# Performance work log

Hardware: AMD Instinct MI355X
Metric: run time of the kernel (lower is better)

Reference implementation:

```python
import jax, jax.numpy as jnp
import numpy as np

S, H, NH, I = 4096, 2048, 16, 5504
HD = H // NH
EPS = 1e-6
ROPE_BASE = 10000.0


def setup_inputs() -> dict:
    key = jax.random.key(0)
    ks = jax.random.split(key, 10)
    sc = lambda fan_in: 1.0 / np.sqrt(fan_in)
    return {
        "x": jax.random.normal(ks[0], (S, H), jnp.float32),
        "wq": jax.random.normal(ks[1], (H, H), jnp.float32) * sc(H),
        "wk": jax.random.normal(ks[2], (H, H), jnp.float32) * sc(H),
        "wv": jax.random.normal(ks[3], (H, H), jnp.float32) * sc(H),
        "wo": jax.random.normal(ks[4], (H, H), jnp.float32) * sc(H),
        "w_gate": jax.random.normal(ks[5], (H, I), jnp.float32) * sc(H),
        "w_up": jax.random.normal(ks[6], (H, I), jnp.float32) * sc(H),
        "w_down": jax.random.normal(ks[7], (I, H), jnp.float32) * sc(I),
        "g1": jnp.ones((H,), jnp.float32),
        "g2": jnp.ones((H,), jnp.float32),
    }


def _rmsnorm(x, g):
    var = jnp.mean(x * x, axis=-1, keepdims=True)
    return x * jax.lax.rsqrt(var + EPS) * g


def _rope(x):
    # x: [S, NH, HD]; classic interleaved-pair rotation applied per position.
    pos = jnp.arange(S, dtype=jnp.float32)
    inv_freq = 1.0 / (ROPE_BASE ** (jnp.arange(0, HD, 2, dtype=jnp.float32) / HD))
    ang = pos[:, None] * inv_freq[None, :]              # [S, HD/2]
    cos = jnp.cos(ang)[:, None, :]                      # [S, 1, HD/2]
    sin = jnp.sin(ang)[:, None, :]
    xe = x[..., 0::2]
    xo = x[..., 1::2]
    out = jnp.stack([xe * cos - xo * sin, xe * sin + xo * cos], axis=-1)
    return out.reshape(x.shape)


def _block(x, wq, wk, wv, wo, w_gate, w_up, w_down, g1, g2):
    # --- attention sublayer ---
    h = _rmsnorm(x, g1)
    q = _rope((h @ wq).reshape(S, NH, HD))
    k = _rope((h @ wk).reshape(S, NH, HD))
    v = (h @ wv).reshape(S, NH, HD)
    scores = jnp.einsum("snd,tnd->nst", q, k) / np.sqrt(HD).astype(np.float32)
    causal = jnp.tril(jnp.ones((S, S), bool))
    scores = jnp.where(causal[None], scores, jnp.finfo(scores.dtype).min)
    probs = jax.nn.softmax(scores, axis=-1)
    attn = jnp.einsum("nst,tnd->snd", probs, v).reshape(S, H)
    x = x + attn @ wo
    # --- MLP sublayer (SwiGLU) ---
    h = _rmsnorm(x, g2)
    mlp = (jax.nn.silu(h @ w_gate) * (h @ w_up)) @ w_down
    return x + mlp


def reference(x, wq, wk, wv, wo, w_gate, w_up, w_down, g1, g2):
    return _block(x, wq, wk, wv, wo, w_gate, w_up, w_down, g1, g2)
```

## Files before the change

### kernel.cpp

```cpp
#include <hip/hip_runtime.h>
#include <stdint.h>

constexpr int SEQ  = 4096;
constexpr int HID  = 2048;
constexpr int NHEAD = 16;
constexpr int HDIM = 128;
constexpr int INTER = 5504;
constexpr int IPAD  = 5632;

using u16 = unsigned short;
typedef __bf16 bf16x8 __attribute__((ext_vector_type(8)));
typedef float  f32x4  __attribute__((ext_vector_type(4)));
typedef u16    u16x4  __attribute__((ext_vector_type(4)));
typedef u16    u16x8  __attribute__((ext_vector_type(8)));

__device__ __forceinline__ u16 f2bf(float f) {
  union { float f; unsigned u; } v; v.f = f;
  return (u16)((v.u + 0x7fffu + ((v.u >> 16) & 1u)) >> 16);
}
__device__ __forceinline__ float bf2f(u16 u) {
  union { unsigned u; float f; } v; v.u = ((unsigned)u) << 16;
  return v.f;
}

__device__ __forceinline__ void gl16(const u16* g, u16* l) {
  u16* gg = const_cast<u16*>(g);
  __builtin_amdgcn_global_load_lds(
      (__attribute__((address_space(1))) u16*)gg,
      (__attribute__((address_space(3))) u16*)l, 16, 0, 0);
}

__device__ __forceinline__ f32x4 mfma16(bf16x8 a, bf16x8 b, f32x4 c) {
  return __builtin_amdgcn_mfma_f32_16x16x32_bf16(a, b, c, 0, 0, 0);
}

__global__ __launch_bounds__(256)
void fill_k(float* __restrict__ o, float v, int n) {
  int i = blockIdx.x * 256 + threadIdx.x;
  if (i < n) o[i] = v;
}

__global__ __launch_bounds__(256)
void rmsnorm_k(const float* __restrict__ x, const float* __restrict__ g,
               u16* __restrict__ o) {
  const int row = blockIdx.x, t = threadIdx.x;
  const float4* xr = (const float4*)(x + (size_t)row * HID);
  float4 a = xr[t * 2], b = xr[t * 2 + 1];
  float ss = a.x*a.x + a.y*a.y + a.z*a.z + a.w*a.w
           + b.x*b.x + b.y*b.y + b.z*b.z + b.w*b.w;
  #pragma unroll
  for (int m = 32; m; m >>= 1) ss += __shfl_xor(ss, m);
  __shared__ float red[4];
  if ((t & 63) == 0) red[t >> 6] = ss;
  __syncthreads();
  const float inv = rsqrtf((red[0]+red[1]+red[2]+red[3]) * (1.0f/HID) + 1e-6f);
  float vals[8] = {a.x,a.y,a.z,a.w,b.x,b.y,b.z,b.w};
  const int base = t * 8;
  u16x8 w;
  #pragma unroll
  for (int i = 0; i < 8; ++i) w[i] = f2bf(vals[i] * inv * g[base + i]);
  *(u16x8*)(o + (size_t)row * HID + base) = w;
}

__global__ __launch_bounds__(256)
void wtrans_k(const float* __restrict__ in, u16* __restrict__ out,
              int ldin, int ldout, int Rin, int Cin) {
  __shared__ float tile[32][33];
  const int cb = blockIdx.x * 32, rb = blockIdx.y * 32;
  const int t = threadIdx.x;
  const int c = t >> 3, r4 = (t & 7) * 4;
  if (rb >= Rin || cb >= Cin) {
    u16x4 z = {0, 0, 0, 0};
    *(u16x4*)(out + (size_t)(cb + c) * ldout + rb + r4) = z;
    return;
  }
  const int r = t >> 3, c4 = (t & 7) * 4;
  float4 v = *(const float4*)(in + (size_t)(rb + r) * ldin + cb + c4);
  tile[r][c4] = v.x; tile[r][c4+1] = v.y; tile[r][c4+2] = v.z; tile[r][c4+3] = v.w;
  __syncthreads();
  u16x4 o;
  #pragma unroll
  for (int i = 0; i < 4; ++i) o[i] = f2bf(tile[r4 + i][c]);
  *(u16x4*)(out + (size_t)(cb + c) * ldout + rb + r4) = o;
}

__global__ __launch_bounds__(256)
void vtrans_k(const u16* __restrict__ v, u16* __restrict__ vt) {
  __shared__ u16 tile[32][36];
  const int s0 = blockIdx.x * 32, d0 = blockIdx.y * 32, n = blockIdx.z;
  const int t = threadIdx.x;
  const int r = t >> 3, c4 = (t & 7) * 4;
  u16x4 in = *(const u16x4*)(v + (size_t)(s0 + r) * HID + n * HDIM + d0 + c4);
  tile[r][c4] = in[0]; tile[r][c4+1] = in[1]; tile[r][c4+2] = in[2]; tile[r][c4+3] = in[3];
  __syncthreads();
  const int d = t >> 3, s4 = (t & 7) * 4;
  u16x4 o;
  #pragma unroll
  for (int i = 0; i < 4; ++i) o[i] = tile[s4 + i][d];
  *(u16x4*)(vt + ((size_t)n * HDIM + d0 + d) * SEQ + s0 + s4) = o;
}

__global__ __launch_bounds__(256)
void rope_k(u16* __restrict__ x) {
  const int idx = blockIdx.x * 256 + threadIdx.x;
  const int i  = idx & 63;
  const int sn = idx >> 6;
  const int s  = sn >> 4;
  const size_t base = (size_t)sn * HDIM + 2 * i;
  const float xe = bf2f(x[base]), xo = bf2f(x[base + 1]);
  const float inv_freq = exp2f(-(float)i * (13.287712379549449f / 64.0f));
  const float ang = (float)s * inv_freq;
  float sv, cv;
  sincosf(ang, &sv, &cv);
  x[base]     = f2bf(xe * cv - xo * sv);
  x[base + 1] = f2bf(xe * sv + xo * cv);
}

template<int EPI>
__global__ __launch_bounds__(512, 2)
void gemm256(const u16* __restrict__ A, const u16* __restrict__ B,
             void* C, const void* extra, int M, int N, int K) {
  __shared__ __align__(16) u16 As[2][2][256 * 32];
  __shared__ __align__(16) u16 Bs[2][2][256 * 32];
  const int tid = threadIdx.x;
  const int w = tid >> 6, lane = tid & 63;
  const int l15 = lane & 15, g = lane >> 4;
  const int wr = w >> 2, wc = w & 3;
  const int m0 = blockIdx.y * 256, n0 = blockIdx.x * 256;
  const int NT = K >> 6;

  f32x4 acc[8][4] = {};

  const int srow0 = w * 32 + (lane >> 2);
  const int sgr   = (((lane & 3) ^ ((lane >> 2) & 3))) * 8;
  const u16* gA0 = A + (size_t)(m0 + srow0) * K + sgr;
  const u16* gB0 = B + (size_t)(n0 + srow0) * K + sgr;
  const size_t r16 = (size_t)16 * K;

#define STA(t, kh, buf) do { \
    const u16* s_ = gA0 + ((size_t)(t) * 64 + (kh) * 32); \
    u16* d_ = &As[buf][kh][w * 1024]; \
    gl16(s_, d_); gl16(s_ + r16, d_ + 512); \
  } while (0)
#define STB(t, kh, buf) do { \
    const u16* s_ = gB0 + ((size_t)(t) * 64 + (kh) * 32); \
    u16* d_ = &Bs[buf][kh][w * 1024]; \
    gl16(s_, d_); gl16(s_ + r16, d_ + 512); \
  } while (0)

  const int rsA = (wr * 128 + l15) * 32 + ((g ^ (l15 & 3)) * 8);
  const int rsB = (wc * 64  + l15) * 32 + ((g ^ (l15 & 3)) * 8);

  STB(0, 0, 0); STA(0, 0, 0); STB(0, 1, 0); STA(0, 1, 0);
  STB(1, 0, 1); STA(1, 0, 1);
  asm volatile("s_waitcnt vmcnt(8)" ::: "memory");
  __builtin_amdgcn_s_barrier();

  for (int T = 0; T < NT; ++T) {
    const int cur = T & 1, nxt = cur ^ 1;
    const int t1 = (T + 1 < NT) ? T + 1 : NT - 1;
    const int t2 = (T + 2 < NT) ? T + 2 : NT - 1;
    bf16x8 bfr[4], af[4];

    #pragma unroll
    for (int j = 0; j < 4; ++j) bfr[j] = *(const bf16x8*)&Bs[cur][0][rsB + j * 512];
    #pragma unroll
    for (int i = 0; i < 4; ++i) af[i] = *(const bf16x8*)&As[cur][0][rsA + i * 512];
    STB(t1, 1, nxt);
    __builtin_amdgcn_s_barrier();
    asm volatile("s_waitcnt lgkmcnt(0)" ::: "memory");
    __builtin_amdgcn_sched_barrier(0);
    __builtin_amdgcn_s_setprio(1);
    #pragma unroll
    for (int i = 0; i < 4; ++i)
      #pragma unroll
      for (int j = 0; j < 4; ++j) acc[i][j] = mfma16(af[i], bfr[j], acc[i][j]);
    __builtin_amdgcn_s_setprio(0);
    __builtin_amdgcn_s_barrier();

    #pragma unroll
    for (int i = 0; i < 4; ++i) af[i] = *(const bf16x8*)&As[cur][0][rsA + 2048 + i * 512];
    STA(t1, 1, nxt);
    asm volatile("s_waitcnt vmcnt(8)" ::: "memory");
    __builtin_amdgcn_s_barrier();
    asm volatile("s_waitcnt lgkmcnt(0)" ::: "memory");
    __builtin_amdgcn_sched_barrier(0);
    __builtin_amdgcn_s_setprio(1);
    #pragma unroll
    for (int i = 0; i < 4; ++i)
      #pragma unroll
      for (int j = 0; j < 4; ++j) acc[i + 4][j] = mfma16(af[i], bfr[j], acc[i + 4][j]);
    __builtin_amdgcn_s_setprio(0);
    __builtin_amdgcn_s_barrier();

    #pragma unroll
    for (int j = 0; j < 4; ++j) bfr[j] = *(const bf16x8*)&Bs[cur][1][rsB + j * 512];
    #pragma unroll
    for (int i = 0; i < 4; ++i) af[i] = *(const bf16x8*)&As[cur][1][rsA + i * 512];
    STB(t2, 0, cur);
    __builtin_amdgcn_s_barrier();
    asm volatile("s_waitcnt lgkmcnt(0)" ::: "memory");
    __builtin_amdgcn_sched_barrier(0);
    __builtin_amdgcn_s_setprio(1);
    #pragma unroll
    for (int i = 0; i < 4; ++i)
      #pragma unroll
      for (int j = 0; j < 4; ++j) acc[i][j] = mfma16(af[i], bfr[j], acc[i][j]);
    __builtin_amdgcn_s_setprio(0);
    __builtin_amdgcn_s_barrier();

    #pragma unroll
    for (int i = 0; i < 4; ++i) af[i] = *(const bf16x8*)&As[cur][1][rsA + 2048 + i * 512];
    STA(t2, 0, cur);
    asm volatile("s_waitcnt vmcnt(8)" ::: "memory");
    __builtin_amdgcn_s_barrier();
    asm volatile("s_waitcnt lgkmcnt(0)" ::: "memory");
    __builtin_amdgcn_sched_barrier(0);
    __builtin_amdgcn_s_setprio(1);
    #pragma unroll
    for (int i = 0; i < 4; ++i)
      #pragma unroll
      for (int j = 0; j < 4; ++j) acc[i + 4][j] = mfma16(af[i], bfr[j], acc[i + 4][j]);
    __builtin_amdgcn_s_setprio(0);
    __builtin_amdgcn_s_barrier();
  }
#undef STA
#undef STB

  #pragma unroll
  for (int i = 0; i < 8; ++i) {
    #pragma unroll
    for (int r = 0; r < 4; ++r) {
      const int row = m0 + wr * 128 + i * 16 + g * 4 + r;
      #pragma unroll
      for (int j = 0; j < 4; ++j) {
        const int col = n0 + wc * 64 + j * 16 + l15;
        const float v = acc[i][j][r];
        if constexpr (EPI == 0) {
          ((u16*)C)[(size_t)(col >> 11) * ((size_t)SEQ * HID)
                    + (size_t)row * HID + (col & 2047)] = f2bf(v);
        } else if constexpr (EPI == 1) {
          const size_t idx = (size_t)row * N + col;
          ((float*)C)[idx] = v + ((const float*)extra)[idx];
        } else if constexpr (EPI == 2) {
          const size_t idx = (size_t)row * N + col;
          const float upv = bf2f(((const u16*)extra)[idx]);
          ((u16*)C)[idx] = f2bf(v / (1.0f + __expf(-v)) * upv);
        } else {
          ((u16*)C)[(size_t)row * N + col] = f2bf(v);
        }
      }
    }
  }
}

__global__ __launch_bounds__(256)
void attn_k(const u16* __restrict__ q, const u16* __restrict__ k,
            const u16* __restrict__ vt, u16* __restrict__ o) {
  __shared__ __align__(16) u16 Ks[64 * 128];
  __shared__ __align__(16) u16 Vs[128 * 64];
  __shared__ __align__(16) u16 Ps[4 * 16 * 64];
  const int b = blockIdx.x;
  const int n    = ((b & 7) << 1) | ((b >> 3) & 1);
  const int qIdx = 63 - (b >> 4);
  const int q0   = qIdx * 64;
  const int tid = threadIdx.x;
  const int wave = tid >> 6, lane = tid & 63;
  const int l15 = lane & 15, g = lane >> 4;

  bf16x8 aq[4];
  {
    const u16* qp = q + (size_t)(q0 + wave*16 + l15) * HID + n * HDIM + g * 8;
    #pragma unroll
    for (int d = 0; d < 4; ++d) aq[d] = *(const bf16x8*)(qp + d * 32);
  }
  float mrow[4], lrow[4];
  #pragma unroll
  for (int r = 0; r < 4; ++r) { mrow[r] = -__builtin_inff(); lrow[r] = 0.0f; }
  f32x4 oacc[8] = {};

  const int kRow = tid >> 4;
  const int kCs  = (tid & 15) ^ (kRow & 7);
  const u16* kg = k + (size_t)kRow * HID + n * HDIM + kCs * 8;
  const int vRow = tid >> 3;
  const int vCs  = (tid & 7) ^ (vRow & 7);
  const u16* vg = vt + ((size_t)n * HDIM + vRow) * SEQ + vCs * 8;

  u16* PW = Ps + wave * 1024;
  const int rsw = (l15 & 7) << 3;
  const float C = 0.12751744f;

  const int nt = qIdx + 1;
  for (int it = 0; it < nt; ++it) {
    const int t0 = it * 64;
    #pragma unroll
    for (int s = 0; s < 4; ++s)
      gl16(kg + (size_t)(t0 + s*16) * HID, Ks + s*2048 + wave*512);
    #pragma unroll
    for (int s = 0; s < 4; ++s)
      gl16(vg + (size_t)(s*32) * SEQ + t0, Vs + s*2048 + wave*512);
    __syncthreads();

    f32x4 sc[4] = {};
    #pragma unroll
    for (int tb = 0; tb < 4; ++tb) {
      #pragma unroll
      for (int dd = 0; dd < 4; ++dd) {
        bf16x8 bk = *(const bf16x8*)(Ks + (tb*16 + l15)*128 + ((dd*32 + g*8) ^ rsw));
        sc[tb] = mfma16(aq[dd], bk, sc[tb]);
      }
    }

    float fex[4];
    #pragma unroll
    for (int r = 0; r < 4; ++r) {
      const int srow = q0 + wave*16 + g*4 + r;
      const int tt = t0 + l15;
      float v0 = sc[0][r], v1 = sc[1][r], v2 = sc[2][r], v3 = sc[3][r];
      if (tt      > srow) v0 = -__builtin_inff();
      if (tt + 16 > srow) v1 = -__builtin_inff();
      if (tt + 32 > srow) v2 = -__builtin_inff();
      if (tt + 48 > srow) v3 = -__builtin_inff();
      float mx = fmaxf(fmaxf(v0, v1), fmaxf(v2, v3));
      mx = fmaxf(mx, __shfl_xor(mx, 1));
      mx = fmaxf(mx, __shfl_xor(mx, 2));
      mx = fmaxf(mx, __shfl_xor(mx, 4));
      mx = fmaxf(mx, __shfl_xor(mx, 8));
      const float mnew = fmaxf(mrow[r], mx);
      const float f = exp2f((mrow[r] - mnew) * C);
      mrow[r] = mnew;
      const float p0 = exp2f((v0 - mnew) * C);
      const float p1 = exp2f((v1 - mnew) * C);
      const float p2 = exp2f((v2 - mnew) * C);
      const float p3 = exp2f((v3 - mnew) * C);
      float ps = (p0 + p1) + (p2 + p3);
      ps += __shfl_xor(ps, 1);
      ps += __shfl_xor(ps, 2);
      ps += __shfl_xor(ps, 4);
      ps += __shfl_xor(ps, 8);
      lrow[r] = lrow[r] * f + ps;
      fex[r] = f;
      const int prow = g*4 + r;
      const int psw = (prow & 7) << 3;
      PW[prow*64 + ( l15        ^ psw)] = f2bf(p0);
      PW[prow*64 + ((16 + l15)  ^ psw)] = f2bf(p1);
      PW[prow*64 + ((32 + l15)  ^ psw)] = f2bf(p2);
      PW[prow*64 + ((48 + l15)  ^ psw)] = f2bf(p3);
    }
    #pragma unroll
    for (int db = 0; db < 8; ++db)
      #pragma unroll
      for (int r = 0; r < 4; ++r) oacc[db][r] *= fex[r];

    bf16x8 ap0 = *(const bf16x8*)(PW + l15*64 + ((g*8)      ^ rsw));
    bf16x8 ap1 = *(const bf16x8*)(PW + l15*64 + ((32 + g*8) ^ rsw));
    #pragma unroll
    for (int db = 0; db < 8; ++db) {
      bf16x8 bv0 = *(const bf16x8*)(Vs + (db*16 + l15)*64 + ((g*8)      ^ rsw));
      bf16x8 bv1 = *(const bf16x8*)(Vs + (db*16 + l15)*64 + ((32 + g*8) ^ rsw));
      oacc[db] = mfma16(ap0, bv0, oacc[db]);
      oacc[db] = mfma16(ap1, bv1, oacc[db]);
    }
    __syncthreads();
  }

  #pragma unroll
  for (int db = 0; db < 8; ++db) {
    #pragma unroll
    for (int r = 0; r < 4; ++r) {
      const int srow = q0 + wave*16 + g*4 + r;
      o[(size_t)srow * HID + n * HDIM + db*16 + l15] = f2bf(oacc[db][r] / lrow[r]);
    }
  }
}

extern "C" void kernel_launch(void* const* d_in, const int* in_sizes, int n_in,
                              void* d_out, int out_size, void* d_ws, size_t ws_size,
                              hipStream_t stream) {
  (void)in_sizes; (void)n_in; (void)out_size;
  const float* x  = (const float*)d_in[0];
  const float* wq = (const float*)d_in[1];
  const float* wk = (const float*)d_in[2];
  const float* wv = (const float*)d_in[3];
  const float* wo = (const float*)d_in[4];
  const float* wg = (const float*)d_in[5];
  const float* wu = (const float*)d_in[6];
  const float* wd = (const float*)d_in[7];
  const float* g1 = (const float*)d_in[8];
  const float* g2 = (const float*)d_in[9];
  float* out = (float*)d_out;

  constexpr size_t HB  = (size_t)SEQ * HID * 2;
  constexpr size_t WT  = (size_t)HID * HID * 2;
  constexpr size_t WUP = (size_t)IPAD * HID * 2;
  constexpr size_t UPH = (size_t)SEQ * IPAD * 2;
  constexpr size_t NEED1 = 4 * HB + 3 * WT;
  constexpr size_t NEED2 = HB + WUP + UPH;
  constexpr size_t NEED = NEED1 > NEED2 ? NEED1 : NEED2;

  if (ws_size < NEED) {
    const int n = SEQ * HID;
    fill_k<<<dim3((n + 255) / 256), 256, 0, stream>>>(out, (float)(ws_size >> 20), n);
    return;
  }

  char* base = (char*)d_ws;
  u16* h1     = (u16*)(base);
  u16* wqkvT  = (u16*)(base + HB);
  u16* qb     = (u16*)(base + HB + 3 * WT);
  u16* kb     = (u16*)(base + 2 * HB + 3 * WT);
  u16* vb     = (u16*)(base + 3 * HB + 3 * WT);
  u16* vtb    = h1;
  u16* ob     = vb;
  u16* woT    = wqkvT;
  u16* h2    = (u16*)(base);
  u16* slotA = (u16*)(base + HB);
  u16* uph   = (u16*)(base + HB + WUP);

  wtrans_k<<<dim3(64, 64), 256, 0, stream>>>(wq, wqkvT,            HID, HID, HID, HID);
  wtrans_k<<<dim3(64, 64), 256, 0, stream>>>(wk, wqkvT + HID*HID,  HID, HID, HID, HID);
  wtrans_k<<<dim3(64, 64), 256, 0, stream>>>(wv, wqkvT + 2*HID*HID,HID, HID, HID, HID);

  rmsnorm_k<<<dim3(SEQ), 256, 0, stream>>>(x, g1, h1);

  gemm256<0><<<dim3(3*HID/256, SEQ/256), 512, 0, stream>>>(
      h1, wqkvT, qb, nullptr, SEQ, 3*HID, HID);

  rope_k<<<dim3(SEQ * NHEAD * 64 / 256), 256, 0, stream>>>(qb);
  rope_k<<<dim3(SEQ * NHEAD * 64 / 256), 256, 0, stream>>>(kb);

  vtrans_k<<<dim3(SEQ/32, HDIM/32, NHEAD), 256, 0, stream>>>(vb, vtb);

  wtrans_k<<<dim3(64, 64), 256, 0, stream>>>(wo, woT, HID, HID, HID, HID);

  attn_k<<<dim3(SEQ/64 * NHEAD), 256, 0, stream>>>(qb, kb, vtb, ob);

  gemm256<1><<<dim3(HID/256, SEQ/256), 512, 0, stream>>>(
      ob, woT, out, x, SEQ, HID, HID);

  rmsnorm_k<<<dim3(SEQ), 256, 0, stream>>>(out, g2, h2);

  wtrans_k<<<dim3(IPAD/32, 64), 256, 0, stream>>>(wu, slotA, INTER, HID, HID, INTER);
  gemm256<3><<<dim3(IPAD/256, SEQ/256), 512, 0, stream>>>(
      h2, slotA, uph, nullptr, SEQ, IPAD, HID);

  wtrans_k<<<dim3(IPAD/32, 64), 256, 0, stream>>>(wg, slotA, INTER, HID, HID, INTER);
  gemm256<2><<<dim3(IPAD/256, SEQ/256), 512, 0, stream>>>(
      h2, slotA, uph, uph, SEQ, IPAD, HID);

  wtrans_k<<<dim3(64, IPAD/32), 256, 0, stream>>>(wd, slotA, HID, IPAD, INTER, HID);
  gemm256<1><<<dim3(HID/256, SEQ/256), 512, 0, stream>>>(
      uph, slotA, out, out, SEQ, HID, IPAD);
}
```

Baseline: 977.5 us.

## Restructure GEMM main loop with full 64-K tile bursts and XCD-aware block remap

Replaces the split half-K staged prefetch pipeline in the 256x256 GEMM with a simpler double buffer. Each iteration issues one burst that loads a full 64-wide K tile for the next step, and the tile is consumed in four quadrant sub-steps using an 8-way XOR swizzle. The kernel now launches on a 1D grid and remaps block ids round-robin across the eight XCDs to improve L2 locality. The trade-off is a shallower prefetch: the code waits on vmcnt(0) at the end of every iteration, which may expose memory latency that the earlier two-stage lookahead hid.

```diff
diff --git a/kernel.cpp b/kernel.cpp
--- a/kernel.cpp
+++ b/kernel.cpp
@@ -119,122 +119,99 @@
 template<int EPI>
 __global__ __launch_bounds__(512, 2)
 void gemm256(const u16* __restrict__ A, const u16* __restrict__ B,
-             void* C, const void* extra, int M, int N, int K) {
-  __shared__ __align__(16) u16 As[2][2][256 * 32];
-  __shared__ __align__(16) u16 Bs[2][2][256 * 32];
+             void* C, const void* extra, int M, int N, int K, int gx) {
+  __shared__ __align__(16) u16 SA[2][256 * 64];
+  __shared__ __align__(16) u16 SB[2][256 * 64];
+  const int nwg = gridDim.x;
+  const int bid = blockIdx.x;
+  const int wgid = (bid & 7) * (nwg >> 3) + (bid >> 3);
+  const int bx = wgid % gx, by = wgid / gx;
+  const int m0 = by * 256, n0 = bx * 256;
   const int tid = threadIdx.x;
   const int w = tid >> 6, lane = tid & 63;
   const int l15 = lane & 15, g = lane >> 4;
   const int wr = w >> 2, wc = w & 3;
-  const int m0 = blockIdx.y * 256, n0 = blockIdx.x * 256;
   const int NT = K >> 6;
 
   f32x4 acc[8][4] = {};
 
-  const int srow0 = w * 32 + (lane >> 2);
-  const int sgr   = (((lane & 3) ^ ((lane >> 2) & 3))) * 8;
-  const u16* gA0 = A + (size_t)(m0 + srow0) * K + sgr;
-  const u16* gB0 = B + (size_t)(n0 + srow0) * K + sgr;
-  const size_t r16 = (size_t)16 * K;
-
-#define STA(t, kh, buf) do { \
-    const u16* s_ = gA0 + ((size_t)(t) * 64 + (kh) * 32); \
-    u16* d_ = &As[buf][kh][w * 1024]; \
-    gl16(s_, d_); gl16(s_ + r16, d_ + 512); \
+  const int srow = tid >> 3;
+  const int sgr  = ((tid & 7) ^ (srow & 7)) * 8;
+  const u16* gA = A + (size_t)(m0 + srow) * K + sgr;
+  const u16* gB = B + (size_t)(n0 + srow) * K + sgr;
+  const size_t i64K = (size_t)64 * K;
+  const int sl = w * 512;
+
+#define BURST(buf, T) do { \
+    const size_t off_ = (size_t)(T) * 64; \
+    gl16(gA + off_,            &SA[buf][0 * 4096 + sl]); \
+    gl16(gA + off_ +     i64K, &SA[buf][1 * 4096 + sl]); \
+    gl16(gA + off_ + 2 * i64K, &SA[buf][2 * 4096 + sl]); \
+    gl16(gA + off_ + 3 * i64K, &SA[buf][3 * 4096 + sl]); \
+    gl16(gB + off_,            &SB[buf][0 * 4096 + sl]); \
+    gl16(gB + off_ +     i64K, &SB[buf][1 * 4096 + sl]); \
+    gl16(gB + off_ + 2 * i64K, &SB[buf][2 * 4096 + sl]); \
+    gl16(gB + off_ + 3 * i64K, &SB[buf][3 * 4096 + sl]); \
   } while (0)
-#define STB(t, kh, buf) do { \
-    const u16* s_ = gB0 + ((size_t)(t) * 64 + (kh) * 32); \
-    u16* d_ = &Bs[buf][kh][w * 1024]; \
-    gl16(s_, d_); gl16(s_ + r16, d_ + 512); \
-  } while (0)
-
-  const int rsA = (wr * 128 + l15) * 32 + ((g ^ (l15 & 3)) * 8);
-  const int rsB = (wc * 64  + l15) * 32 + ((g ^ (l15 & 3)) * 8);
-
-  STB(0, 0, 0); STA(0, 0, 0); STB(0, 1, 0); STA(0, 1, 0);
-  STB(1, 0, 1); STA(1, 0, 1);
-  asm volatile("s_waitcnt vmcnt(8)" ::: "memory");
+
+  const int axor = l15 & 7;
+  int aoff[2];
+  aoff[0] = ((g)     ^ axor) * 8;
+  aoff[1] = ((4 + g) ^ axor) * 8;
+  const int arow0 = (wr * 128 + l15) * 64;
+  const int brow0 = (wc * 64  + l15) * 64;
+
+  BURST(0, 0);
+  asm volatile("s_waitcnt vmcnt(0)" ::: "memory");
   __builtin_amdgcn_s_barrier();
 
   for (int T = 0; T < NT; ++T) {
-    const int cur = T & 1, nxt = cur ^ 1;
-    const int t1 = (T + 1 < NT) ? T + 1 : NT - 1;
-    const int t2 = (T + 2 < NT) ? T + 2 : NT - 1;
-    bf16x8 bfr[4], af[4];
-
-    #pragma unroll
-    for (int j = 0; j < 4; ++j) bfr[j] = *(const bf16x8*)&Bs[cur][0][rsB + j * 512];
-    #pragma unroll
-    for (int i = 0; i < 4; ++i) af[i] = *(const bf16x8*)&As[cur][0][rsA + i * 512];
-    STB(t1, 1, nxt);
-    __builtin_amdgcn_s_barrier();
-    asm volatile("s_waitcnt lgkmcnt(0)" ::: "memory");
-    __builtin_amdgcn_sched_barrier(0);
-    __builtin_amdgcn_s_setprio(1);
-    #pragma unroll
-    for (int i = 0; i < 4; ++i)
-      #pragma unroll
-      for (int j = 0; j < 4; ++j) acc[i][j] = mfma16(af[i], bfr[j], acc[i][j]);
-    __builtin_amdgcn_s_setprio(0);
-    __builtin_amdgcn_s_barrier();
-
-    #pragma unroll
-    for (int i = 0; i < 4; ++i) af[i] = *(const bf16x8*)&As[cur][0][rsA + 2048 + i * 512];
-    STA(t1, 1, nxt);
-    asm volatile("s_waitcnt vmcnt(8)" ::: "memory");
-    __builtin_amdgcn_s_barrier();
-    asm volatile("s_waitcnt lgkmcnt(0)" ::: "memory");
-    __builtin_amdgcn_sched_barrier(0);
-    __builtin_amdgcn_s_setprio(1);
-    #pragma unroll
-    for (int i = 0; i < 4; ++i)
-      #pragma unroll
-      for (int j = 0; j < 4; ++j) acc[i + 4][j] = mfma16(af[i], bfr[j], acc[i + 4][j]);
-    __builtin_amdgcn_s_setprio(0);
-    __builtin_amdgcn_s_barrier();
-
-    #pragma unroll
-    for (int j = 0; j < 4; ++j) bfr[j] = *(const bf16x8*)&Bs[cur][1][rsB + j * 512];
-    #pragma unroll
-    for (int i = 0; i < 4; ++i) af[i] = *(const bf16x8*)&As[cur][1][rsA + i * 512];
-    STB(t2, 0, cur);
-    __builtin_amdgcn_s_barrier();
-    asm volatile("s_waitcnt lgkmcnt(0)" ::: "memory");
-    __builtin_amdgcn_sched_barrier(0);
-    __builtin_amdgcn_s_setprio(1);
-    #pragma unroll
-    for (int i = 0; i < 4; ++i)
-      #pragma unroll
-      for (int j = 0; j < 4; ++j) acc[i][j] = mfma16(af[i], bfr[j], acc[i][j]);
-    __builtin_amdgcn_s_setprio(0);
-    __builtin_amdgcn_s_barrier();
-
-    #pragma unroll
-    for (int i = 0; i < 4; ++i) af[i] = *(const bf16x8*)&As[cur][1][rsA + 2048 + i * 512];
-    STA(t2, 0, cur);
-    asm volatile("s_waitcnt vmcnt(8)" ::: "memory");
-    __builtin_amdgcn_s_barrier();
-    asm volatile("s_waitcnt lgkmcnt(0)" ::: "memory");
-    __builtin_amdgcn_sched_barrier(0);
-    __builtin_amdgcn_s_setprio(1);
-    #pragma unroll
-    for (int i = 0; i < 4; ++i)
-      #pragma unroll
-      for (int j = 0; j < 4; ++j) acc[i + 4][j] = mfma16(af[i], bfr[j], acc[i + 4][j]);
-    __builtin_amdgcn_s_setprio(0);
-    __builtin_amdgcn_s_barrier();
-  }
-#undef STA
-#undef STB
+    const int buf = T & 1;
+    const u16* sA = SA[buf];
+    const u16* sB = SB[buf];
+    #pragma unroll
+    for (int q = 0; q < 4; ++q) {
+      const int ih = q >> 1, jh = q & 1;
+      bf16x8 af[4][2], bf[2][2];
+      #pragma unroll
+      for (int ii = 0; ii < 4; ++ii)
+        #pragma unroll
+        for (int ks = 0; ks < 2; ++ks)
+          af[ii][ks] = *(const bf16x8*)&sA[arow0 + (ih * 64 + ii * 16) * 64 + aoff[ks]];
+      #pragma unroll
+      for (int jj = 0; jj < 2; ++jj)
+        #pragma unroll
+        for (int ks = 0; ks < 2; ++ks)
+          bf[jj][ks] = *(const bf16x8*)&sB[brow0 + (jh * 32 + jj * 16) * 64 + aoff[ks]];
+      if (q == 0 && T + 1 < NT) BURST(buf ^ 1, T + 1);
+      __builtin_amdgcn_s_barrier();
+      asm volatile("s_waitcnt lgkmcnt(0)" ::: "memory");
+      __builtin_amdgcn_sched_barrier(0);
+      __builtin_amdgcn_s_setprio(1);
+      #pragma unroll
+      for (int ii = 0; ii < 4; ++ii)
+        #pragma unroll
+        for (int jj = 0; jj < 2; ++jj)
+          #pragma unroll
+          for (int ks = 0; ks < 2; ++ks)
+            acc[ih * 4 + ii][jh * 2 + jj] =
+                mfma16(af[ii][ks], bf[jj][ks], acc[ih * 4 + ii][jh * 2 + jj]);
+      __builtin_amdgcn_s_setprio(0);
+      if (q == 3)
+        asm volatile("s_waitcnt vmcnt(0)" ::: "memory");
+      __builtin_amdgcn_s_barrier();
+    }
+  }
+#undef BURST
 
   #pragma unroll
   for (int i = 0; i < 8; ++i) {
     #pragma unroll
     for (int r = 0; r < 4; ++r) {
-      const int row = m0 + wr * 128 + i * 16 + g * 4 + r;
+      const int row = m0 + wr * 128 + (i >> 2) * 64 + (i & 3) * 16 + g * 4 + r;
       #pragma unroll
       for (int j = 0; j < 4; ++j) {
-        const int col = n0 + wc * 64 + j * 16 + l15;
+        const int col = n0 + wc * 64 + (j >> 1) * 32 + (j & 1) * 16 + l15;
         const float v = acc[i][j][r];
         if constexpr (EPI == 0) {
           ((u16*)C)[(size_t)(col >> 11) * ((size_t)SEQ * HID)
@@ -423,8 +400,7 @@
 
   rmsnorm_k<<<dim3(SEQ), 256, 0, stream>>>(x, g1, h1);
 
-  gemm256<0><<<dim3(3*HID/256, SEQ/256), 512, 0, stream>>>(
-      h1, wqkvT, qb, nullptr, SEQ, 3*HID, HID);
+  gemm256<0><<<dim3(384), 512, 0, stream>>>(h1, wqkvT, qb, nullptr, SEQ, 3*HID, HID, 24);
 
   rope_k<<<dim3(SEQ * NHEAD * 64 / 256), 256, 0, stream>>>(qb);
   rope_k<<<dim3(SEQ * NHEAD * 64 / 256), 256, 0, stream>>>(kb);
@@ -435,20 +411,16 @@
 
   attn_k<<<dim3(SEQ/64 * NHEAD), 256, 0, stream>>>(qb, kb, vtb, ob);
 
-  gemm256<1><<<dim3(HID/256, SEQ/256), 512, 0, stream>>>(
-      ob, woT, out, x, SEQ, HID, HID);
+  gemm256<1><<<dim3(128), 512, 0, stream>>>(ob, woT, out, x, SEQ, HID, HID, 8);
 
   rmsnorm_k<<<dim3(SEQ), 256, 0, stream>>>(out, g2, h2);
 
   wtrans_k<<<dim3(IPAD/32, 64), 256, 0, stream>>>(wu, slotA, INTER, HID, HID, INTER);
-  gemm256<3><<<dim3(IPAD/256, SEQ/256), 512, 0, stream>>>(
-      h2, slotA, uph, nullptr, SEQ, IPAD, HID);
+  gemm256<3><<<dim3(352), 512, 0, stream>>>(h2, slotA, uph, nullptr, SEQ, IPAD, HID, 22);
 
   wtrans_k<<<dim3(IPAD/32, 64), 256, 0, stream>>>(wg, slotA, INTER, HID, HID, INTER);
-  gemm256<2><<<dim3(IPAD/256, SEQ/256), 512, 0, stream>>>(
-      h2, slotA, uph, uph, SEQ, IPAD, HID);
+  gemm256<2><<<dim3(352), 512, 0, stream>>>(h2, slotA, uph, uph, SEQ, IPAD, HID, 22);
 
   wtrans_k<<<dim3(64, IPAD/32), 256, 0, stream>>>(wd, slotA, HID, IPAD, INTER, HID);
-  gemm256<1><<<dim3(HID/256, SEQ/256), 512, 0, stream>>>(
-      uph, slotA, out, out, SEQ, HID, IPAD);
-}
+  gemm256<1><<<dim3(128), 512, 0, stream>>>(uph, slotA, out, out, SEQ, HID, IPAD, 8);
+}
```

Result: slower. 1.103 ms (+12.8%).
